# Kernel optimization log

Hardware: AMD Instinct MI355X
Metric: run time of the kernel (lower is better)

The kernel has to match this reference:

```python
import jax, jax.numpy as jnp
import numpy as np

T_STEPS = 4
LAYERS = 10
CYCLE = 10
C = 64
TAU = 1.2
V_TH = 0.5
SG_ALPHA = 4.0  # spikingjelly default surrogate.Sigmoid alpha


@jax.custom_vjp
def heaviside_sg(x):
    return (x >= 0.0).astype(x.dtype)

def _h_fwd(x):
    return heaviside_sg(x), x

def _h_bwd(x, g):
    s = jax.nn.sigmoid(SG_ALPHA * x)
    return (SG_ALPHA * s * (1.0 - s) * g,)

heaviside_sg.defvjp(_h_fwd, _h_bwd)


def lif(x_seq):
    # MultiStepLIFNode: v' = v + (x - (v - v_reset))/tau, hard reset to v_reset=0,
    # detach_reset=True -> spike in reset path is stop-gradient'ed.
    def step(v, x):
        v = v + (x - v) / TAU
        spike = heaviside_sg(v - V_TH)
        v = v * (1.0 - jax.lax.stop_gradient(spike))
        return v, spike
    _, spikes = jax.lax.scan(step, jnp.zeros_like(x_seq[0]), x_seq)
    return spikes


def conv_seq(x, w, b, dilation=1):
    # x: [T,B,Cin,L]; w: [Cout,Cin,K]; 'same' padding for odd K
    T, B, Ci, L = x.shape
    K = w.shape[-1]
    pad = (K - 1) * dilation // 2
    y = jax.lax.conv_general_dilated(
        x.reshape(T * B, Ci, L), w, (1,), [(pad, pad)],
        rhs_dilation=(dilation,), dimension_numbers=('NCH', 'OIH', 'NCH'))
    y = y + b[None, :, None]
    return y.reshape(T, B, -1, L)


def setup_inputs() -> dict:
    key = jax.random.key(0)
    ks = jax.random.split(key, 20)
    B, L = 4, 4096
    s = 0.1
    n = jax.random.normal
    inp = {
        'audio': jax.random.uniform(ks[0], (B, L), dtype=jnp.float32),
        'diffusion_step': jax.random.randint(ks[1], (B,), 0, 50),
        'W_in': n(ks[2], (C, 1, 1), jnp.float32) * s,
        'b_in': n(ks[3], (C,), jnp.float32) * s,
        'demb_w1': n(ks[4], (LAYERS, C, 1), jnp.float32) * s,
        'demb_b1': n(ks[5], (LAYERS, C), jnp.float32) * s,
        'demb_w2': n(ks[6], (LAYERS, C, C), jnp.float32) * s,
        'demb_b2': n(ks[7], (LAYERS, C), jnp.float32) * s,
        'dproj_w': n(ks[8], (LAYERS, C, C), jnp.float32) * s,
        'dproj_b': n(ks[9], (LAYERS, C), jnp.float32) * s,
        'conv_w': n(ks[10], (LAYERS, 2 * C, C, 3), jnp.float32) * 0.05,
        'conv_b': n(ks[11], (LAYERS, 2 * C), jnp.float32) * s,
        'skip_w': n(ks[12], (LAYERS, C, C, 1), jnp.float32) * s,
        'skip_b': n(ks[13], (LAYERS, C), jnp.float32) * s,
        'res_w': n(ks[14], (LAYERS, C, C, 1), jnp.float32) * s,
        'res_b': n(ks[15], (LAYERS, C), jnp.float32) * s,
        'W_out': n(ks[16], (1, C, 1), jnp.float32) * s,
        'b_out': n(ks[17], (1,), jnp.float32) * s,
    }
    return inp


def reference(audio, diffusion_step, W_in, b_in, demb_w1, demb_b1, demb_w2,
              demb_b2, dproj_w, dproj_b, conv_w, conv_b, skip_w, skip_b,
              res_w, res_b, W_out, b_out):
    B, L = audio.shape
    # Poisson encoder: spike = 1[u < x] per timestep (fixed key -> deterministic)
    u = jax.random.uniform(jax.random.key(42), (T_STEPS, B, 1, L), dtype=jnp.float32)
    spike_seq = (u < audio[None, :, None, :]).astype(jnp.float32)

    x = conv_seq(spike_seq, W_in, b_in)          # [T,B,C,L]
    x = lif(x)

    d = diffusion_step.astype(jnp.float32)[:, None]  # [B,1]
    total_skip = jnp.zeros_like(x)
    for i in range(LAYERS):
        dilation = 2 ** (i % CYCLE)
        emb = jax.nn.silu(d @ demb_w1[i].T + demb_b1[i]) @ demb_w2[i].T + demb_b2[i]  # [B,C]
        proj = emb @ dproj_w[i].T + dproj_b[i]                                        # [B,C]
        y = x + proj[None, :, :, None]
        y = conv_seq(y, conv_w[i], conv_b[i], dilation=dilation)  # [T,B,2C,L]
        y = lif(y)
        gate, filt = jnp.split(y, 2, axis=2)
        y = jax.nn.sigmoid(gate) * jnp.tanh(filt)
        total_skip = total_skip + conv_seq(y, skip_w[i], skip_b[i])
        x = x + conv_seq(y, res_w[i], res_b[i])

    total_skip = jax.nn.relu(total_skip)
    out = conv_seq(total_skip, W_out, b_out)  # [T,B,1,L]
    out = lif(out)
    return out.sum(axis=0)  # [B,1,L]
```

## Files before the change

### kernel.cpp

```cpp
#include <hip/hip_runtime.h>

#define LL 4096
#define NB 4
#define NC 64
#define NT 4
#define NLAYERS 10
#define XS 5120
#define XPAD 512

typedef float v2f __attribute__((ext_vector_type(2)));

__device__ __forceinline__ void threefry2x32(unsigned x0, unsigned x1,
                                             unsigned& o0, unsigned& o1) {
  const unsigned ks0 = 0u, ks1 = 42u;
  const unsigned ks2 = 0x1BD11BDAu ^ ks0 ^ ks1;
  const unsigned ks[3] = {ks0, ks1, ks2};
  const unsigned r0[4] = {13u, 15u, 26u, 6u};
  const unsigned r1[4] = {17u, 29u, 16u, 24u};
  x0 += ks0; x1 += ks1;
#pragma unroll
  for (int g = 0; g < 5; ++g) {
    const unsigned* rr = (g & 1) ? r1 : r0;
#pragma unroll
    for (int j = 0; j < 4; ++j) {
      x0 += x1;
      unsigned r = rr[j];
      x1 = (x1 << r) | (x1 >> (32u - r));
      x1 ^= x0;
    }
    x0 += ks[(g + 1) % 3];
    x1 += ks[(g + 2) % 3] + (unsigned)(g + 1);
  }
  o0 = x0; o1 = x1;
}

__device__ __forceinline__ float u01(unsigned bits) {
  return __uint_as_float((bits >> 9) | 0x3f800000u) - 1.0f;
}

__device__ __forceinline__ float lif_step(float& v, float xt) {
  v = v + (xt - v) / 1.2f;
  float s = (v >= 0.5f) ? 1.0f : 0.0f;
  v = v * (1.0f - s);
  return s;
}

__global__ void prep_kernel(const float* __restrict__ skip_w,
                            const float* __restrict__ res_w,
                            const float* __restrict__ conv_w,
                            float* __restrict__ skipT,
                            float* __restrict__ resT,
                            float* __restrict__ wT) {
  int i = blockIdx.x;
  for (int idx = threadIdx.x; idx < 4096; idx += 256) {
    int c = idx >> 6, cp = idx & 63;
    skipT[i * 4096 + cp * 64 + c] = skip_w[i * 4096 + c * 64 + cp];
    resT[i * 4096 + cp * 64 + c] = res_w[i * 4096 + c * 64 + cp];
  }
  for (int idx = threadIdx.x; idx < 8 * 64 * 3 * 16; idx += 256) {
    int col = idx & 15;
    int r = idx >> 4;
    int k = r % 3; r /= 3;
    int ci = r % 64;
    int g = r / 64;
    int co = (col < 8) ? (g * 8 + col) : (64 + g * 8 + (col - 8));
    wT[i * 24576 + idx] = conv_w[(i * 128 + co) * 192 + ci * 3 + k];
  }
}

__global__ void proj_kernel(const int* __restrict__ dstep,
                            const float* __restrict__ w1, const float* __restrict__ b1,
                            const float* __restrict__ w2, const float* __restrict__ b2,
                            const float* __restrict__ pw, const float* __restrict__ pb,
                            float* __restrict__ proj) {
  __shared__ float e1[NB][NC];
  __shared__ float e2[NB][NC];
  int i = blockIdx.x;
  int tid = threadIdx.x;
  int b = tid >> 6, c = tid & 63;
  float d = (float)dstep[b];
  float v = d * w1[i * 64 + c] + b1[i * 64 + c];
  v = v / (1.0f + expf(-v));
  e1[b][c] = v;
  __syncthreads();
  float a = b2[i * 64 + c];
  for (int cp = 0; cp < 64; ++cp) a += e1[b][cp] * w2[(i * 64 + c) * 64 + cp];
  e2[b][c] = a;
  __syncthreads();
  float p = pb[i * 64 + c];
  for (int cp = 0; cp < 64; ++cp) p += e2[b][cp] * pw[(i * 64 + c) * 64 + cp];
  proj[(i * 4 + b) * 64 + c] = p;
}

__global__ void pc_kernel(const float* __restrict__ proj,
                          const float* __restrict__ conv_w,
                          float* __restrict__ pc) {
  __shared__ float pv[64];
  int layer = blockIdx.x, b = blockIdx.y;
  int tid = threadIdx.x;
  if (tid < 64) pv[tid] = proj[(layer * 4 + b) * 64 + tid];
  __syncthreads();
  int co = tid;
  const float* w = conv_w + (layer * 128 + co) * 192;
  float s0 = 0.0f, s1 = 0.0f, s2 = 0.0f;
  for (int ci = 0; ci < 64; ++ci) {
    float p = pv[ci];
    s0 += p * w[ci * 3 + 0];
    s1 += p * w[ci * 3 + 1];
    s2 += p * w[ci * 3 + 2];
  }
  float* o = pc + ((layer * 4 + b) * 128 + co) * 3;
  o[0] = s0; o[1] = s1; o[2] = s2;
}

__global__ void padzero_kernel(float* __restrict__ x) {
  int row = blockIdx.x;
  float* base = x + (size_t)row * XS * 4;
  for (int i = threadIdx.x; i < XPAD; i += 256) {
    *(float4*)&base[i * 4] = float4{0.f, 0.f, 0.f, 0.f};
    *(float4*)&base[(XPAD + LL + i) * 4] = float4{0.f, 0.f, 0.f, 0.f};
  }
}

__global__ void encode_lif_kernel(const float* __restrict__ audio,
                                  const float* __restrict__ W_in,
                                  const float* __restrict__ b_in,
                                  float* __restrict__ x) {
  int tid = threadIdx.x;
  int lq = tid & 63, grp = tid >> 6;
  int l = blockIdx.x * 64 + lq;
  int b = blockIdx.y;
  float a = audio[b * LL + l];
  unsigned p0 = (unsigned)(b * LL + l);
  unsigned p1 = 16384u + p0;
  unsigned o00, o01, o10, o11;
  threefry2x32(p0, p0 + 32768u, o00, o01);
  threefry2x32(p1, p1 + 32768u, o10, o11);
  float sp[4];
  sp[0] = (u01(o00) < a) ? 1.0f : 0.0f;
  sp[1] = (u01(o10) < a) ? 1.0f : 0.0f;
  sp[2] = (u01(o01) < a) ? 1.0f : 0.0f;
  sp[3] = (u01(o11) < a) ? 1.0f : 0.0f;
  for (int j = 0; j < 16; ++j) {
    int c = grp * 16 + j;
    float w = W_in[c], bb = b_in[c];
    float v = 0.0f;
    float4 o;
    float* op = (float*)&o;
#pragma unroll
    for (int t = 0; t < 4; ++t) op[t] = lif_step(v, w * sp[t] + bb);
    *(float4*)&x[(size_t)((b * 64 + c) * XS + XPAD + l) * 4] = o;
  }
}

template <int DIL>
__global__ __launch_bounds__(256) void layer_conv_kernel(
    const float* __restrict__ x, const float* __restrict__ wT,
    const float* __restrict__ conv_b, const float* __restrict__ pc,
    float* __restrict__ y, int layer) {
  int tid = threadIdx.x;
  int g = blockIdx.y;
  int b = blockIdx.z;
  int l = blockIdx.x * 256 + tid;
  const float* wbase = wT + (size_t)(layer * 8 + g) * 3072;

  const float* px = x + (size_t)(b * 64 * XS + XPAD + l) * 4;

  v2f ag[16], af[16];
#pragma unroll
  for (int q = 0; q < 16; ++q) {
    ag[q] = (v2f)(0.0f);
    af[q] = (v2f)(0.0f);
  }

  float4 xa[3], xb[3];
  auto loadx = [&](float4* dst) {
    dst[0] = *(const float4*)(px - (size_t)DIL * 4);
    dst[1] = *(const float4*)px;
    dst[2] = *(const float4*)(px + (size_t)DIL * 4);
    px += (size_t)XS * 4;
  };
  auto compute = [&](int ci, const float4* xv) {
#pragma unroll
    for (int k = 0; k < 3; ++k) {
      const v2f* wr = (const v2f*)&wbase[(ci * 3 + k) * 16];
      v2f g0 = wr[0], g1 = wr[1], g2 = wr[2], g3 = wr[3];
      v2f f0 = wr[4], f1 = wr[5], f2 = wr[6], f3 = wr[7];
      const float* xk = (const float*)&xv[k];
#pragma unroll
      for (int t = 0; t < 4; ++t) {
        float xq = xk[t];
        v2f x2;
        x2.x = xq; x2.y = xq;
        ag[t * 4 + 0] += g0 * x2;
        ag[t * 4 + 1] += g1 * x2;
        ag[t * 4 + 2] += g2 * x2;
        ag[t * 4 + 3] += g3 * x2;
        af[t * 4 + 0] += f0 * x2;
        af[t * 4 + 1] += f1 * x2;
        af[t * 4 + 2] += f2 * x2;
        af[t * 4 + 3] += f3 * x2;
      }
    }
  };

  loadx(xa);
  for (int ci = 0; ci < 64; ci += 2) {
    loadx(xb);
    compute(ci, xa);
    if (ci + 2 < 64) loadx(xa);
    compute(ci + 1, xb);
  }

  const float SIG1 = 0.73105857863000489f;
  const float TANH1 = 0.76159415595576486f;
  bool lb = (l < DIL), rb = (l >= LL - DIL);
#pragma unroll
  for (int j = 0; j < 8; ++j) {
    int cog = g * 8 + j;
    int cof = 64 + g * 8 + j;
    const float* pg = pc + ((layer * 4 + b) * 128 + cog) * 3;
    const float* pf = pc + ((layer * 4 + b) * 128 + cof) * 3;
    float S0g = pg[0], S1g = pg[1], S2g = pg[2];
    float S0f = pf[0], S1f = pf[1], S2f = pf[2];
    float bg = conv_b[layer * 128 + cog] + S0g + S1g + S2g;
    float bf = conv_b[layer * 128 + cof] + S0f + S1f + S2f;
    bg -= (lb ? S0g : 0.0f) + (rb ? S2g : 0.0f);
    bf -= (lb ? S0f : 0.0f) + (rb ? S2f : 0.0f);
    float vg = 0.0f, vf = 0.0f;
    float4 o;
    float* op = (float*)&o;
#pragma unroll
    for (int t = 0; t < 4; ++t) {
      float av = ag[t * 4 + (j >> 1)][j & 1];
      float fv = af[t * 4 + (j >> 1)][j & 1];
      float sg = lif_step(vg, av + bg);
      float sf = lif_step(vf, fv + bf);
      float gv = (sg != 0.0f) ? SIG1 : 0.5f;
      float tv = (sf != 0.0f) ? TANH1 : 0.0f;
      op[t] = gv * tv;
    }
    *(float4*)&y[(size_t)((b * 64 + cog) * LL + l) * 4] = o;
  }
}

__global__ __launch_bounds__(256) void skip_res_kernel(
    const float* __restrict__ y, const float* __restrict__ skipT,
    const float* __restrict__ resT, const float* __restrict__ skip_b,
    const float* __restrict__ res_b, float* __restrict__ tskip,
    float* __restrict__ x, int layer) {
  int tid = threadIdx.x;
  int lg = tid & 31;
  int cg = tid >> 5;
  int cv = blockIdx.y;
  int b = blockIdx.z;
  int l0 = blockIdx.x * 64 + lg * 2;
  int c0 = cg * 8;

  const float* wsrc = (cv ? resT : skipT) + layer * 4096 + c0;
  const float* yb = y + (size_t)(b * 64 * LL + l0) * 4;

  v2f acc[32];
#pragma unroll
  for (int q = 0; q < 32; ++q) acc[q] = (v2f)(0.0f);

  float4 w0a = *(const float4*)&wsrc[0];
  float4 w1a = *(const float4*)&wsrc[4];
  float4 y0a = *(const float4*)yb;
  float4 y1a = *(const float4*)(yb + 4);

  for (int cp = 0; cp < 64; ++cp) {
    int cpn = (cp < 63) ? cp + 1 : 63;
    float4 w0b = *(const float4*)&wsrc[cpn * 64];
    float4 w1b = *(const float4*)&wsrc[cpn * 64 + 4];
    float4 y0b = *(const float4*)(yb + (size_t)cpn * LL * 4);
    float4 y1b = *(const float4*)(yb + (size_t)cpn * LL * 4 + 4);

    float wv[8] = {w0a.x, w0a.y, w0a.z, w0a.w, w1a.x, w1a.y, w1a.z, w1a.w};
    const v2f* yp0 = (const v2f*)&y0a;
    const v2f* yp1 = (const v2f*)&y1a;
#pragma unroll
    for (int i = 0; i < 8; ++i) {
      v2f w2;
      w2.x = wv[i]; w2.y = wv[i];
      acc[i * 4 + 0] += w2 * yp0[0];
      acc[i * 4 + 1] += w2 * yp0[1];
      acc[i * 4 + 2] += w2 * yp1[0];
      acc[i * 4 + 3] += w2 * yp1[1];
    }
    w0a = w0b; w1a = w1b; y0a = y0b; y1a = y1b;
  }

  const float* bsrc = (cv ? res_b : skip_b) + layer * 64 + c0;
#pragma unroll
  for (int i = 0; i < 8; ++i) {
    float bb = bsrc[i];
    float r[8];
#pragma unroll
    for (int q = 0; q < 4; ++q) {
      r[q * 2 + 0] = acc[i * 4 + q][0] + bb;
      r[q * 2 + 1] = acc[i * 4 + q][1] + bb;
    }
    if (cv == 0) {
      size_t idx = (size_t)((b * 64 + c0 + i) * LL + l0) * 4;
      float4 o0, o1;
      if (layer == 0) {
        o0 = float4{0.f, 0.f, 0.f, 0.f};
        o1 = o0;
      } else {
        o0 = *(const float4*)&tskip[idx];
        o1 = *(const float4*)&tskip[idx + 4];
      }
      o0.x += r[0]; o0.y += r[1]; o0.z += r[2]; o0.w += r[3];
      o1.x += r[4]; o1.y += r[5]; o1.z += r[6]; o1.w += r[7];
      *(float4*)&tskip[idx] = o0;
      *(float4*)&tskip[idx + 4] = o1;
    } else {
      size_t idx = (size_t)((b * 64 + c0 + i) * XS + XPAD + l0) * 4;
      float4 o0 = *(const float4*)&x[idx];
      float4 o1 = *(const float4*)&x[idx + 4];
      o0.x += r[0]; o0.y += r[1]; o0.z += r[2]; o0.w += r[3];
      o1.x += r[4]; o1.y += r[5]; o1.z += r[6]; o1.w += r[7];
      *(float4*)&x[idx] = o0;
      *(float4*)&x[idx + 4] = o1;
    }
  }
}

__global__ void out_kernel(const float* __restrict__ tskip,
                           const float* __restrict__ W_out,
                           const float* __restrict__ b_out,
                           float* __restrict__ out) {
  __shared__ float red[4][4][64];
  int tid = threadIdx.x;
  int lq = tid & 63, grp = tid >> 6;
  int l = blockIdx.x * 64 + lq;
  int b = blockIdx.y;
  float acc[4] = {0.0f, 0.0f, 0.0f, 0.0f};
  for (int j = 0; j < 16; ++j) {
    int c = grp * 16 + j;
    float w = W_out[c];
    float4 sv = *(const float4*)&tskip[(size_t)((b * 64 + c) * LL + l) * 4];
    acc[0] += fmaxf(sv.x, 0.0f) * w;
    acc[1] += fmaxf(sv.y, 0.0f) * w;
    acc[2] += fmaxf(sv.z, 0.0f) * w;
    acc[3] += fmaxf(sv.w, 0.0f) * w;
  }
#pragma unroll
  for (int t = 0; t < 4; ++t) red[grp][t][lq] = acc[t];
  __syncthreads();
  if (grp == 0) {
    float bo = b_out[0];
    float v = 0.0f, s = 0.0f;
#pragma unroll
    for (int t = 0; t < 4; ++t) {
      float a = red[0][t][lq] + red[1][t][lq] + red[2][t][lq] + red[3][t][lq] + bo;
      s += lif_step(v, a);
    }
    out[b * LL + l] = s;
  }
}

extern "C" void kernel_launch(void* const* d_in, const int* in_sizes, int n_in,
                              void* d_out, int out_size, void* d_ws, size_t ws_size,
                              hipStream_t stream) {
  const float* audio   = (const float*)d_in[0];
  const int*   dstep   = (const int*)d_in[1];
  const float* W_in    = (const float*)d_in[2];
  const float* b_in    = (const float*)d_in[3];
  const float* demb_w1 = (const float*)d_in[4];
  const float* demb_b1 = (const float*)d_in[5];
  const float* demb_w2 = (const float*)d_in[6];
  const float* demb_b2 = (const float*)d_in[7];
  const float* dproj_w = (const float*)d_in[8];
  const float* dproj_b = (const float*)d_in[9];
  const float* conv_w  = (const float*)d_in[10];
  const float* conv_b  = (const float*)d_in[11];
  const float* skip_w  = (const float*)d_in[12];
  const float* skip_b  = (const float*)d_in[13];
  const float* res_w   = (const float*)d_in[14];
  const float* res_b   = (const float*)d_in[15];
  const float* W_out   = (const float*)d_in[16];
  const float* b_out   = (const float*)d_in[17];
  float* out = (float*)d_out;
  float* ws = (float*)d_ws;

  float* proj  = ws;
  float* skipT = proj + 2560;
  float* resT  = skipT + 40960;
  float* pc    = resT + 40960;
  float* wT    = pc + 15360;
  float* x     = wT + 245760;
  float* y     = x + 5242880;
  float* tskip = y + 4194304;

  prep_kernel<<<10, 256, 0, stream>>>(skip_w, res_w, conv_w, skipT, resT, wT);
  proj_kernel<<<10, 256, 0, stream>>>(dstep, demb_w1, demb_b1, demb_w2, demb_b2,
                                      dproj_w, dproj_b, proj);
  pc_kernel<<<dim3(10, 4), 128, 0, stream>>>(proj, conv_w, pc);
  padzero_kernel<<<256, 256, 0, stream>>>(x);
  encode_lif_kernel<<<dim3(64, 4), 256, 0, stream>>>(audio, W_in, b_in, x);

  for (int i = 0; i < NLAYERS; ++i) {
    dim3 gc(16, 8, 4);
    switch (i) {
      case 0: layer_conv_kernel<1><<<gc, 256, 0, stream>>>(x, wT, conv_b, pc, y, i); break;
      case 1: layer_conv_kernel<2><<<gc, 256, 0, stream>>>(x, wT, conv_b, pc, y, i); break;
      case 2: layer_conv_kernel<4><<<gc, 256, 0, stream>>>(x, wT, conv_b, pc, y, i); break;
      case 3: layer_conv_kernel<8><<<gc, 256, 0, stream>>>(x, wT, conv_b, pc, y, i); break;
      case 4: layer_conv_kernel<16><<<gc, 256, 0, stream>>>(x, wT, conv_b, pc, y, i); break;
      case 5: layer_conv_kernel<32><<<gc, 256, 0, stream>>>(x, wT, conv_b, pc, y, i); break;
      case 6: layer_conv_kernel<64><<<gc, 256, 0, stream>>>(x, wT, conv_b, pc, y, i); break;
      case 7: layer_conv_kernel<128><<<gc, 256, 0, stream>>>(x, wT, conv_b, pc, y, i); break;
      case 8: layer_conv_kernel<256><<<gc, 256, 0, stream>>>(x, wT, conv_b, pc, y, i); break;
      case 9: layer_conv_kernel<512><<<gc, 256, 0, stream>>>(x, wT, conv_b, pc, y, i); break;
    }
    skip_res_kernel<<<dim3(64, 2, 4), 256, 0, stream>>>(y, skipT, resT, skip_b,
                                                        res_b, tskip, x, i);
  }
  out_kernel<<<dim3(64, 4), 256, 0, stream>>>(tskip, W_out, b_out, out);
}
```

Baseline: 878.7 us.

## Split conv input channels across thread halves and shrink skip/res tiles for occupancy

The dilated conv kernel now splits the 64 input channels between two halves of the block. Each half accumulates 32 channels over 128 positions, and the partial sums are combined through shared memory before the LIF/gate epilogue. This doubles the grid. The skip/res kernel's per-thread tile is halved to 4 output channels by 2 positions, which doubles its grid and cuts register pressure. Both changes aim to fill more CUs on the MI355X, at the cost of a shared-memory reduction with barriers, an idle half-block during the epilogue, and more redundant weight and activation loads.

```diff
diff --git a/kernel.cpp b/kernel.cpp
--- a/kernel.cpp
+++ b/kernel.cpp
@@ -158,13 +158,15 @@
     const float* __restrict__ x, const float* __restrict__ wT,
     const float* __restrict__ conv_b, const float* __restrict__ pc,
     float* __restrict__ y, int layer) {
-  int tid = threadIdx.x;
+  __shared__ v2f comb[128 * 17];
+  int tid = threadIdx.x;
+  int lt = tid & 127, h = tid >> 7;
   int g = blockIdx.y;
   int b = blockIdx.z;
-  int l = blockIdx.x * 256 + tid;
+  int l = blockIdx.x * 128 + lt;
   const float* wbase = wT + (size_t)(layer * 8 + g) * 3072;
 
-  const float* px = x + (size_t)(b * 64 * XS + XPAD + l) * 4;
+  const float* px = x + (size_t)((b * 64 + h * 32) * XS + XPAD + l) * 4;
 
   v2f ag[16], af[16];
 #pragma unroll
@@ -204,43 +206,64 @@
     }
   };
 
+  int cib = h * 32;
   loadx(xa);
-  for (int ci = 0; ci < 64; ci += 2) {
+  for (int cl = 0; cl < 32; cl += 2) {
     loadx(xb);
-    compute(ci, xa);
-    if (ci + 2 < 64) loadx(xa);
-    compute(ci + 1, xb);
-  }
-
-  const float SIG1 = 0.73105857863000489f;
-  const float TANH1 = 0.76159415595576486f;
-  bool lb = (l < DIL), rb = (l >= LL - DIL);
-#pragma unroll
-  for (int j = 0; j < 8; ++j) {
-    int cog = g * 8 + j;
-    int cof = 64 + g * 8 + j;
-    const float* pg = pc + ((layer * 4 + b) * 128 + cog) * 3;
-    const float* pf = pc + ((layer * 4 + b) * 128 + cof) * 3;
-    float S0g = pg[0], S1g = pg[1], S2g = pg[2];
-    float S0f = pf[0], S1f = pf[1], S2f = pf[2];
-    float bg = conv_b[layer * 128 + cog] + S0g + S1g + S2g;
-    float bf = conv_b[layer * 128 + cof] + S0f + S1f + S2f;
-    bg -= (lb ? S0g : 0.0f) + (rb ? S2g : 0.0f);
-    bf -= (lb ? S0f : 0.0f) + (rb ? S2f : 0.0f);
-    float vg = 0.0f, vf = 0.0f;
-    float4 o;
-    float* op = (float*)&o;
-#pragma unroll
-    for (int t = 0; t < 4; ++t) {
-      float av = ag[t * 4 + (j >> 1)][j & 1];
-      float fv = af[t * 4 + (j >> 1)][j & 1];
-      float sg = lif_step(vg, av + bg);
-      float sf = lif_step(vf, fv + bf);
-      float gv = (sg != 0.0f) ? SIG1 : 0.5f;
-      float tv = (sf != 0.0f) ? TANH1 : 0.0f;
-      op[t] = gv * tv;
-    }
-    *(float4*)&y[(size_t)((b * 64 + cog) * LL + l) * 4] = o;
+    compute(cib + cl, xa);
+    if (cl + 2 < 32) loadx(xa);
+    compute(cib + cl + 1, xb);
+  }
+
+  if (h == 1) {
+#pragma unroll
+    for (int q = 0; q < 16; ++q) comb[lt * 17 + q] = ag[q];
+  }
+  __syncthreads();
+  if (h == 0) {
+#pragma unroll
+    for (int q = 0; q < 16; ++q) ag[q] += comb[lt * 17 + q];
+  }
+  __syncthreads();
+  if (h == 1) {
+#pragma unroll
+    for (int q = 0; q < 16; ++q) comb[lt * 17 + q] = af[q];
+  }
+  __syncthreads();
+  if (h == 0) {
+#pragma unroll
+    for (int q = 0; q < 16; ++q) af[q] += comb[lt * 17 + q];
+
+    const float SIG1 = 0.73105857863000489f;
+    const float TANH1 = 0.76159415595576486f;
+    bool lb = (l < DIL), rb = (l >= LL - DIL);
+#pragma unroll
+    for (int j = 0; j < 8; ++j) {
+      int cog = g * 8 + j;
+      int cof = 64 + g * 8 + j;
+      const float* pg = pc + ((layer * 4 + b) * 128 + cog) * 3;
+      const float* pf = pc + ((layer * 4 + b) * 128 + cof) * 3;
+      float S0g = pg[0], S1g = pg[1], S2g = pg[2];
+      float S0f = pf[0], S1f = pf[1], S2f = pf[2];
+      float bg = conv_b[layer * 128 + cog] + S0g + S1g + S2g;
+      float bf = conv_b[layer * 128 + cof] + S0f + S1f + S2f;
+      bg -= (lb ? S0g : 0.0f) + (rb ? S2g : 0.0f);
+      bf -= (lb ? S0f : 0.0f) + (rb ? S2f : 0.0f);
+      float vg = 0.0f, vf = 0.0f;
+      float4 o;
+      float* op = (float*)&o;
+#pragma unroll
+      for (int t = 0; t < 4; ++t) {
+        float av = ag[t * 4 + (j >> 1)][j & 1];
+        float fv = af[t * 4 + (j >> 1)][j & 1];
+        float sg = lif_step(vg, av + bg);
+        float sf = lif_step(vf, fv + bf);
+        float gv = (sg != 0.0f) ? SIG1 : 0.5f;
+        float tv = (sf != 0.0f) ? TANH1 : 0.0f;
+        op[t] = gv * tv;
+      }
+      *(float4*)&y[(size_t)((b * 64 + cog) * LL + l) * 4] = o;
+    }
   }
 }
 
@@ -250,37 +273,35 @@
     const float* __restrict__ res_b, float* __restrict__ tskip,
     float* __restrict__ x, int layer) {
   int tid = threadIdx.x;
-  int lg = tid & 31;
-  int cg = tid >> 5;
+  int lg = tid & 15;
+  int cg = tid >> 4;
   int cv = blockIdx.y;
   int b = blockIdx.z;
-  int l0 = blockIdx.x * 64 + lg * 2;
-  int c0 = cg * 8;
+  int l0 = blockIdx.x * 32 + lg * 2;
+  int c0 = cg * 4;
 
   const float* wsrc = (cv ? resT : skipT) + layer * 4096 + c0;
   const float* yb = y + (size_t)(b * 64 * LL + l0) * 4;
 
-  v2f acc[32];
-#pragma unroll
-  for (int q = 0; q < 32; ++q) acc[q] = (v2f)(0.0f);
-
-  float4 w0a = *(const float4*)&wsrc[0];
-  float4 w1a = *(const float4*)&wsrc[4];
+  v2f acc[16];
+#pragma unroll
+  for (int q = 0; q < 16; ++q) acc[q] = (v2f)(0.0f);
+
+  float4 wa = *(const float4*)&wsrc[0];
   float4 y0a = *(const float4*)yb;
   float4 y1a = *(const float4*)(yb + 4);
 
   for (int cp = 0; cp < 64; ++cp) {
     int cpn = (cp < 63) ? cp + 1 : 63;
-    float4 w0b = *(const float4*)&wsrc[cpn * 64];
-    float4 w1b = *(const float4*)&wsrc[cpn * 64 + 4];
+    float4 wb = *(const float4*)&wsrc[cpn * 64];
     float4 y0b = *(const float4*)(yb + (size_t)cpn * LL * 4);
     float4 y1b = *(const float4*)(yb + (size_t)cpn * LL * 4 + 4);
 
-    float wv[8] = {w0a.x, w0a.y, w0a.z, w0a.w, w1a.x, w1a.y, w1a.z, w1a.w};
+    float wv[4] = {wa.x, wa.y, wa.z, wa.w};
     const v2f* yp0 = (const v2f*)&y0a;
     const v2f* yp1 = (const v2f*)&y1a;
 #pragma unroll
-    for (int i = 0; i < 8; ++i) {
+    for (int i = 0; i < 4; ++i) {
       v2f w2;
       w2.x = wv[i]; w2.y = wv[i];
       acc[i * 4 + 0] += w2 * yp0[0];
@@ -288,12 +309,12 @@
       acc[i * 4 + 2] += w2 * yp1[0];
       acc[i * 4 + 3] += w2 * yp1[1];
     }
-    w0a = w0b; w1a = w1b; y0a = y0b; y1a = y1b;
+    wa = wb; y0a = y0b; y1a = y1b;
   }
 
   const float* bsrc = (cv ? res_b : skip_b) + layer * 64 + c0;
 #pragma unroll
-  for (int i = 0; i < 8; ++i) {
+  for (int i = 0; i < 4; ++i) {
     float bb = bsrc[i];
     float r[8];
 #pragma unroll
@@ -402,7 +423,7 @@
   encode_lif_kernel<<<dim3(64, 4), 256, 0, stream>>>(audio, W_in, b_in, x);
 
   for (int i = 0; i < NLAYERS; ++i) {
-    dim3 gc(16, 8, 4);
+    dim3 gc(32, 8, 4);
     switch (i) {
       case 0: layer_conv_kernel<1><<<gc, 256, 0, stream>>>(x, wT, conv_b, pc, y, i); break;
       case 1: layer_conv_kernel<2><<<gc, 256, 0, stream>>>(x, wT, conv_b, pc, y, i); break;
@@ -415,8 +436,8 @@
       case 8: layer_conv_kernel<256><<<gc, 256, 0, stream>>>(x, wT, conv_b, pc, y, i); break;
       case 9: layer_conv_kernel<512><<<gc, 256, 0, stream>>>(x, wT, conv_b, pc, y, i); break;
     }
-    skip_res_kernel<<<dim3(64, 2, 4), 256, 0, stream>>>(y, skipT, resT, skip_b,
-                                                        res_b, tskip, x, i);
+    skip_res_kernel<<<dim3(128, 2, 4), 256, 0, stream>>>(y, skipT, resT, skip_b,
+                                                         res_b, tskip, x, i);
   }
   out_kernel<<<dim3(64, 4), 256, 0, stream>>>(tskip, W_out, b_out, out);
 }
```

New measurement: 1.086 ms. +23.6%, slower.

## Transpose y and tskip to channel-inner layout and fuse skip/res projections

Applied to the files above, without the earlier changes.

Stores the gated activation y and the skip accumulator as [B][L][C][T] instead of [B][C][L][T], and rewrites skip_res_kernel so one block computes both the skip and residual 1x1 convolutions from a single read of y. Previously y was read twice, once per projection (blockIdx.y), so this removes that duplicate traffic. The channel-inner layout makes each thread's per-channel y loads contiguous. In exchange, tskip writes and out_kernel reads become strided across channels, which may reduce coalescing, and the x update keeps the old layout with a different access pattern.

```diff
diff --git a/kernel.cpp b/kernel.cpp
--- a/kernel.cpp
+++ b/kernel.cpp
@@ -240,7 +240,7 @@
       float tv = (sf != 0.0f) ? TANH1 : 0.0f;
       op[t] = gv * tv;
     }
-    *(float4*)&y[(size_t)((b * 64 + cog) * LL + l) * 4] = o;
+    *(float4*)&y[(size_t)((b * LL + l) * 64 + cog) * 4] = o;
   }
 }
 
@@ -250,79 +250,79 @@
     const float* __restrict__ res_b, float* __restrict__ tskip,
     float* __restrict__ x, int layer) {
   int tid = threadIdx.x;
-  int lg = tid & 31;
-  int cg = tid >> 5;
-  int cv = blockIdx.y;
-  int b = blockIdx.z;
-  int l0 = blockIdx.x * 64 + lg * 2;
-  int c0 = cg * 8;
-
-  const float* wsrc = (cv ? resT : skipT) + layer * 4096 + c0;
-  const float* yb = y + (size_t)(b * 64 * LL + l0) * 4;
-
-  v2f acc[32];
-#pragma unroll
-  for (int q = 0; q < 32; ++q) acc[q] = (v2f)(0.0f);
-
-  float4 w0a = *(const float4*)&wsrc[0];
-  float4 w1a = *(const float4*)&wsrc[4];
-  float4 y0a = *(const float4*)yb;
-  float4 y1a = *(const float4*)(yb + 4);
+  int lg = tid & 15;
+  int cg = tid >> 4;
+  int b = blockIdx.y;
+  int l0 = blockIdx.x * 32 + lg * 2;
+  int c0 = cg * 4;
+
+  const float* wS = skipT + layer * 4096 + c0;
+  const float* wR = resT + layer * 4096 + c0;
+  const float* yb = y + (size_t)(b * LL + l0) * 64 * 4;
+
+  v2f aS[16], aR[16];
+#pragma unroll
+  for (int q = 0; q < 16; ++q) { aS[q] = (v2f)(0.0f); aR[q] = (v2f)(0.0f); }
+
+  float4 wSa = *(const float4*)&wS[0];
+  float4 wRa = *(const float4*)&wR[0];
+  float4 y0a = *(const float4*)&yb[0];
+  float4 y1a = *(const float4*)&yb[256];
 
   for (int cp = 0; cp < 64; ++cp) {
     int cpn = (cp < 63) ? cp + 1 : 63;
-    float4 w0b = *(const float4*)&wsrc[cpn * 64];
-    float4 w1b = *(const float4*)&wsrc[cpn * 64 + 4];
-    float4 y0b = *(const float4*)(yb + (size_t)cpn * LL * 4);
-    float4 y1b = *(const float4*)(yb + (size_t)cpn * LL * 4 + 4);
-
-    float wv[8] = {w0a.x, w0a.y, w0a.z, w0a.w, w1a.x, w1a.y, w1a.z, w1a.w};
+    float4 wSb = *(const float4*)&wS[cpn * 64];
+    float4 wRb = *(const float4*)&wR[cpn * 64];
+    float4 y0b = *(const float4*)&yb[cpn * 4];
+    float4 y1b = *(const float4*)&yb[256 + cpn * 4];
+
+    float sv[4] = {wSa.x, wSa.y, wSa.z, wSa.w};
+    float rv[4] = {wRa.x, wRa.y, wRa.z, wRa.w};
     const v2f* yp0 = (const v2f*)&y0a;
     const v2f* yp1 = (const v2f*)&y1a;
 #pragma unroll
-    for (int i = 0; i < 8; ++i) {
-      v2f w2;
-      w2.x = wv[i]; w2.y = wv[i];
-      acc[i * 4 + 0] += w2 * yp0[0];
-      acc[i * 4 + 1] += w2 * yp0[1];
-      acc[i * 4 + 2] += w2 * yp1[0];
-      acc[i * 4 + 3] += w2 * yp1[1];
-    }
-    w0a = w0b; w1a = w1b; y0a = y0b; y1a = y1b;
-  }
-
-  const float* bsrc = (cv ? res_b : skip_b) + layer * 64 + c0;
-#pragma unroll
-  for (int i = 0; i < 8; ++i) {
-    float bb = bsrc[i];
-    float r[8];
-#pragma unroll
-    for (int q = 0; q < 4; ++q) {
-      r[q * 2 + 0] = acc[i * 4 + q][0] + bb;
-      r[q * 2 + 1] = acc[i * 4 + q][1] + bb;
-    }
-    if (cv == 0) {
-      size_t idx = (size_t)((b * 64 + c0 + i) * LL + l0) * 4;
-      float4 o0, o1;
-      if (layer == 0) {
-        o0 = float4{0.f, 0.f, 0.f, 0.f};
-        o1 = o0;
-      } else {
-        o0 = *(const float4*)&tskip[idx];
-        o1 = *(const float4*)&tskip[idx + 4];
-      }
-      o0.x += r[0]; o0.y += r[1]; o0.z += r[2]; o0.w += r[3];
-      o1.x += r[4]; o1.y += r[5]; o1.z += r[6]; o1.w += r[7];
-      *(float4*)&tskip[idx] = o0;
-      *(float4*)&tskip[idx + 4] = o1;
-    } else {
-      size_t idx = (size_t)((b * 64 + c0 + i) * XS + XPAD + l0) * 4;
-      float4 o0 = *(const float4*)&x[idx];
-      float4 o1 = *(const float4*)&x[idx + 4];
-      o0.x += r[0]; o0.y += r[1]; o0.z += r[2]; o0.w += r[3];
-      o1.x += r[4]; o1.y += r[5]; o1.z += r[6]; o1.w += r[7];
-      *(float4*)&x[idx] = o0;
-      *(float4*)&x[idx + 4] = o1;
+    for (int i = 0; i < 4; ++i) {
+      v2f s2, r2;
+      s2.x = sv[i]; s2.y = sv[i];
+      r2.x = rv[i]; r2.y = rv[i];
+      aS[i * 4 + 0] += s2 * yp0[0];
+      aS[i * 4 + 1] += s2 * yp0[1];
+      aS[i * 4 + 2] += s2 * yp1[0];
+      aS[i * 4 + 3] += s2 * yp1[1];
+      aR[i * 4 + 0] += r2 * yp0[0];
+      aR[i * 4 + 1] += r2 * yp0[1];
+      aR[i * 4 + 2] += r2 * yp1[0];
+      aR[i * 4 + 3] += r2 * yp1[1];
+    }
+    wSa = wSb; wRa = wRb; y0a = y0b; y1a = y1b;
+  }
+
+#pragma unroll
+  for (int i = 0; i < 4; ++i) {
+    int c = c0 + i;
+    float sbb = skip_b[layer * 64 + c];
+    float rbb = res_b[layer * 64 + c];
+#pragma unroll
+    for (int dl = 0; dl < 2; ++dl) {
+      v2f p01 = aS[i * 4 + dl * 2 + 0];
+      v2f p23 = aS[i * 4 + dl * 2 + 1];
+      size_t idx = ((size_t)(b * LL + l0 + dl) * 64 + c) * 4;
+      float4 o;
+      if (layer == 0) o = float4{0.f, 0.f, 0.f, 0.f};
+      else o = *(const float4*)&tskip[idx];
+      o.x += p01[0] + sbb; o.y += p01[1] + sbb;
+      o.z += p23[0] + sbb; o.w += p23[1] + sbb;
+      *(float4*)&tskip[idx] = o;
+    }
+#pragma unroll
+    for (int dl = 0; dl < 2; ++dl) {
+      v2f p01 = aR[i * 4 + dl * 2 + 0];
+      v2f p23 = aR[i * 4 + dl * 2 + 1];
+      size_t idx = ((size_t)(b * 64 + c) * XS + XPAD + l0 + dl) * 4;
+      float4 o = *(const float4*)&x[idx];
+      o.x += p01[0] + rbb; o.y += p01[1] + rbb;
+      o.z += p23[0] + rbb; o.w += p23[1] + rbb;
+      *(float4*)&x[idx] = o;
     }
   }
 }
@@ -340,7 +340,7 @@
   for (int j = 0; j < 16; ++j) {
     int c = grp * 16 + j;
     float w = W_out[c];
-    float4 sv = *(const float4*)&tskip[(size_t)((b * 64 + c) * LL + l) * 4];
+    float4 sv = *(const float4*)&tskip[(size_t)((b * LL + l) * 64 + c) * 4];
     acc[0] += fmaxf(sv.x, 0.0f) * w;
     acc[1] += fmaxf(sv.y, 0.0f) * w;
     acc[2] += fmaxf(sv.z, 0.0f) * w;
@@ -415,8 +415,8 @@
       case 8: layer_conv_kernel<256><<<gc, 256, 0, stream>>>(x, wT, conv_b, pc, y, i); break;
       case 9: layer_conv_kernel<512><<<gc, 256, 0, stream>>>(x, wT, conv_b, pc, y, i); break;
     }
-    skip_res_kernel<<<dim3(64, 2, 4), 256, 0, stream>>>(y, skipT, resT, skip_b,
-                                                        res_b, tskip, x, i);
+    skip_res_kernel<<<dim3(128, 4), 256, 0, stream>>>(y, skipT, resT, skip_b,
+                                                      res_b, tskip, x, i);
   }
   out_kernel<<<dim3(64, 4), 256, 0, stream>>>(tskip, W_out, b_out, out);
 }
```

Result: slower. 1.123 ms (+27.8%).
